# Kernel optimization log

Measured on AMD Instinct MI355X. Metric: run time of the kernel, lower is better.

## Reference

```python
import jax, jax.numpy as jnp
import numpy as np

D = 512      # node_feature_size
LAT = 768    # latent_size
B = 16       # number of graphs
S = 256      # conditioning sequence length
H = 8        # attention heads


def _ln(x, g, b):
    m = x.mean(-1, keepdims=True)
    v = jnp.var(x, axis=-1, keepdims=True)
    return (x - m) / jnp.sqrt(v + 1e-5) * g + b


def setup_inputs() -> dict:
    key = jax.random.key(0)
    ks = jax.random.split(key, 10)
    lengths = np.array([512 + 32 * i for i in range(B)])  # ragged node counts
    N = int(lengths.sum())                                # 12032
    Lmax = int(lengths.max())                             # 992
    graph_batch = jnp.asarray(np.repeat(np.arange(B), lengths), dtype=jnp.int32)
    valid = np.array([S - 8 * i for i in range(B)])
    # torch key_padding_mask semantics: True = position is ignored (padding)
    conditioning_mask = jnp.asarray(np.arange(S)[None, :] >= valid[:, None])
    p = lambda k, sh: jax.random.normal(k, sh, jnp.float32) * 0.02
    return dict(
        graph_nodes=jax.random.normal(ks[0], (N, D), jnp.float32),
        graph_batch=graph_batch,
        conditioning_vector=jax.random.normal(ks[1], (B, S, LAT), jnp.float32),
        conditioning_mask=conditioning_mask,
        max_nodes=Lmax,
        num_heads=H,
        Wq=p(ks[2], (D, D)), bq=jnp.zeros(D, jnp.float32),
        Wk=p(ks[3], (LAT, D)), bk=jnp.zeros(D, jnp.float32),
        Wv=p(ks[4], (LAT, D)), bv=jnp.zeros(D, jnp.float32),
        in_w=p(ks[5], (3, D, D)), in_b=jnp.zeros((3, D), jnp.float32),
        Wo=p(ks[6], (D, D)), bo=jnp.zeros(D, jnp.float32),
        ln1_g=jnp.ones(D, jnp.float32), ln1_b=jnp.zeros(D, jnp.float32),
        W1=p(ks[7], (D, D)), b1=jnp.zeros(D, jnp.float32),
        ln2_g=jnp.ones(D, jnp.float32), ln2_b=jnp.zeros(D, jnp.float32),
    )


def reference(graph_nodes, graph_batch, conditioning_vector, conditioning_mask,
              max_nodes, num_heads, Wq, bq, Wk, bk, Wv, bv, in_w, in_b,
              Wo, bo, ln1_g, ln1_b, W1, b1, ln2_g, ln2_b):
    N, Dm = graph_nodes.shape
    Bn, Sk, _ = conditioning_vector.shape
    dh = Dm // num_heads
    # --- pad ragged node sets to dense [B, Lmax, D] (vectorized scatter) ---
    counts = jax.ops.segment_sum(jnp.ones(N, jnp.int32), graph_batch, num_segments=Bn)
    starts = jnp.concatenate([jnp.zeros(1, jnp.int32), jnp.cumsum(counts)[:-1].astype(jnp.int32)])
    pos = jnp.arange(N, dtype=jnp.int32) - starts[graph_batch]
    dense = jnp.zeros((Bn, max_nodes, Dm), graph_nodes.dtype).at[graph_batch, pos].set(graph_nodes)
    # --- projections ---
    q = dense @ Wq + bq
    k = conditioning_vector @ Wk + bk
    v = conditioning_vector @ Wv + bv
    # --- MultiheadAttention internal in-projections ---
    qh = (q @ in_w[0] + in_b[0]).reshape(Bn, max_nodes, num_heads, dh)
    kh = (k @ in_w[1] + in_b[1]).reshape(Bn, Sk, num_heads, dh)
    vh = (v @ in_w[2] + in_b[2]).reshape(Bn, Sk, num_heads, dh)
    scores = jnp.einsum('blhd,bshd->bhls', qh, kh) / jnp.sqrt(jnp.asarray(dh, qh.dtype))
    scores = jnp.where(conditioning_mask[:, None, None, :], -jnp.inf, scores)
    attn = jax.nn.softmax(scores, axis=-1)     # [B,H,L,S]
    av_attn = attn.mean(axis=1)                # head-averaged weights [B,L,S]
    ctx = jnp.einsum('bhls,bshd->blhd', attn, vh).reshape(Bn, max_nodes, Dm)
    attn_out = ctx @ Wo + bo
    # --- residual + LN + FFN + LN (dropout inactive / eval mode) ---
    x = _ln(attn_out + dense, ln1_g, ln1_b)
    x = jax.nn.leaky_relu(x @ W1 + b1) + x     # slope 0.01 matches nn.LeakyReLU
    x = _ln(x, ln2_g, ln2_b)
    # --- unpad back to ragged [N, D] (vectorized gather) ---
    node_out = x[graph_batch, pos]
    return node_out, av_attn
```

## Files before the change

kernel.cpp:

```cpp
#include <hip/hip_runtime.h>
#include <math.h>

#define D_   512
#define LAT_ 768
#define B_   16
#define S_   256
#define H_   8
#define DH_  64

typedef __bf16 bf16x8 __attribute__((ext_vector_type(8)));
typedef float f32x4 __attribute__((ext_vector_type(4)));

__device__ __forceinline__ unsigned short f2bf(float f) {
  unsigned u = __float_as_uint(f);
  unsigned r = (u + 0x7fffu + ((u >> 16) & 1u)) >> 16;
  return (unsigned short)r;
}

__global__ void mask_canon_k(const void* __restrict__ mask, int* __restrict__ out, int n) {
  int i = blockIdx.x * blockDim.x + threadIdx.x;
  if (i >= n) return;
  const unsigned char* pb = (const unsigned char*)mask;
  const int*   pi = (const int*)mask;
  const float* pf = (const float*)mask;
  unsigned int w = ((const unsigned int*)mask)[1023];
  int v;
  if (w == 0x01010101u)      v = pb[i];
  else if (w == 0x3f800000u) v = (pf[i] != 0.0f);
  else                       v = (pi[i] != 0);
  out[i] = v ? 1 : 0;
}

__global__ void starts_k(const int* __restrict__ gb, int* __restrict__ starts, int n) {
  int i = blockIdx.x * blockDim.x + threadIdx.x;
  if (i >= n) return;
  if (i == 0 || gb[i] != gb[i - 1]) starts[gb[i]] = i;
}

__global__ __launch_bounds__(256) void scatter_k(const float* __restrict__ nodes,
    const int* __restrict__ gb, const int* __restrict__ starts,
    float* __restrict__ dense, int Lmax) {
  int i = blockIdx.x;
  int b = gb[i], p = i - starts[b];
  const float* src = nodes + (size_t)i * D_;
  float* dst = dense + ((size_t)b * Lmax + p) * D_;
  dst[threadIdx.x]       = src[threadIdx.x];
  dst[threadIdx.x + 256] = src[threadIdx.x + 256];
}

__device__ __forceinline__ void pack_chunk(const float* __restrict__ W,
    unsigned short* __restrict__ out, int K, int ntoff, int idx) {
  int n = idx & 511, kc = idx >> 9;
  int kt = kc >> 2, kblk = kc & 3;
  int nt = n >> 7, nblk = (n >> 4) & 7, col = n & 15;
  int KT = K >> 5;
  size_t ob = ((size_t)((nt + ntoff) * KT + kt) * 4096) + nblk * 512 + kblk * 128 + col * 8;
  unsigned short v[8];
#pragma unroll
  for (int j = 0; j < 8; ++j) v[j] = f2bf(W[(size_t)(kc * 8 + j) * 512 + n]);
  int4 pk;
  pk.x = v[0] | (v[1] << 16); pk.y = v[2] | (v[3] << 16);
  pk.z = v[4] | (v[5] << 16); pk.w = v[6] | (v[7] << 16);
  *(int4*)&out[ob] = pk;
}

__global__ __launch_bounds__(256) void pack1_k(const float* __restrict__ in_w,
    const float* __restrict__ Wo, const float* __restrict__ W1,
    unsigned short* iw0, unsigned short* iw1, unsigned short* iw2,
    unsigned short* Wo_pk, unsigned short* W1_pk) {
  int bid = blockIdx.x, sel = bid >> 7, within = bid & 127;
  const float* W; unsigned short* out;
  switch (sel) {
    case 0: W = in_w;               out = iw0;   break;
    case 1: W = in_w + 512 * 512;   out = iw1;   break;
    case 2: W = in_w + 2 * 512 * 512; out = iw2; break;
    case 3: W = Wo;                 out = Wo_pk; break;
    default: W = W1;                out = W1_pk; break;
  }
  pack_chunk(W, out, 512, 0, within * 256 + threadIdx.x);
}

__global__ __launch_bounds__(256) void pack2_k(const float* __restrict__ Wqp,
    const float* __restrict__ Wkp, const float* __restrict__ Wvp,
    unsigned short* Wqp_pk, unsigned short* kv_pk) {
  int bid = blockIdx.x, tid = threadIdx.x;
  if (bid < 128)      pack_chunk(Wqp, Wqp_pk, 512, 0, bid * 256 + tid);
  else if (bid < 320) pack_chunk(Wkp, kv_pk, 768, 0, (bid - 128) * 256 + tid);
  else                pack_chunk(Wvp, kv_pk, 768, 4, (bid - 320) * 256 + tid);
}

__device__ __forceinline__ void mgemm64(const float* __restrict__ A,
    const unsigned short* __restrict__ Bpk, const float* __restrict__ bias,
    float* __restrict__ C, int M, int N, int K, int xt, int yt,
    unsigned short* Al, unsigned short* Bl) {
  const int tid = threadIdx.x;
  const int lane = tid & 63, wid = tid >> 6;
  const int wr = wid >> 1, wc = wid & 1;
  const int row0 = yt * 64, col0 = xt * 128;
  const int KT = K >> 5;
  f32x4 acc[2][4];
#pragma unroll
  for (int m = 0; m < 2; ++m)
#pragma unroll
    for (int n = 0; n < 4; ++n) acc[m][n] = (f32x4){0.f, 0.f, 0.f, 0.f};
  const int kb0 = tid & 3, ar = tid >> 2;
  const unsigned short* bsrc = Bpk + (size_t)xt * KT * 4096;

  for (int kt = 0; kt < KT; ++kt) {
    {
      const unsigned short* g1 = bsrc + (size_t)kt * 4096 + wid * 512 + lane * 8;
      __builtin_amdgcn_global_load_lds(
          (const __attribute__((address_space(1))) void*)g1,
          (__attribute__((address_space(3))) void*)&Bl[wid * 512], 16, 0, 0);
      __builtin_amdgcn_global_load_lds(
          (const __attribute__((address_space(1))) void*)(g1 + 2048),
          (__attribute__((address_space(3))) void*)&Bl[2048 + wid * 512], 16, 0, 0);
    }
    {
      const float* ap = A + (size_t)(row0 + ar) * K + kt * 32 + kb0 * 8;
      float4 f0 = *(const float4*)ap;
      float4 f1 = *(const float4*)(ap + 4);
      int4 pk;
      pk.x = f2bf(f0.x) | (f2bf(f0.y) << 16);
      pk.y = f2bf(f0.z) | (f2bf(f0.w) << 16);
      pk.z = f2bf(f1.x) | (f2bf(f1.y) << 16);
      pk.w = f2bf(f1.z) | (f2bf(f1.w) << 16);
      *(int4*)&Al[(ar >> 4) * 512 + kb0 * 128 + (ar & 15) * 8] = pk;
    }
    __syncthreads();
    bf16x8 af[2], bfr[4];
#pragma unroll
    for (int m = 0; m < 2; ++m)
      af[m] = *(const bf16x8*)&Al[(wr * 2 + m) * 512 + lane * 8];
#pragma unroll
    for (int n = 0; n < 4; ++n)
      bfr[n] = *(const bf16x8*)&Bl[(wc * 4 + n) * 512 + lane * 8];
#pragma unroll
    for (int m = 0; m < 2; ++m)
#pragma unroll
      for (int n = 0; n < 4; ++n)
        acc[m][n] = __builtin_amdgcn_mfma_f32_16x16x32_bf16(af[m], bfr[n], acc[m][n], 0, 0, 0);
    __syncthreads();
  }
  const int cl = lane & 15, rg = lane >> 4;
  float bv[4];
#pragma unroll
  for (int n = 0; n < 4; ++n)
    bv[n] = bias ? bias[col0 + wc * 64 + n * 16 + cl] : 0.f;
#pragma unroll
  for (int m = 0; m < 2; ++m) {
    int r = row0 + wr * 32 + m * 16 + rg * 4;
#pragma unroll
    for (int n = 0; n < 4; ++n) {
      int c = col0 + wc * 64 + n * 16 + cl;
#pragma unroll
      for (int i = 0; i < 4; ++i)
        C[(size_t)(r + i) * N + c] = acc[m][n][i] + bv[n];
    }
  }
}

__global__ __launch_bounds__(256) void gemm64_k(const float* __restrict__ A,
    const unsigned short* __restrict__ Bpk, const float* __restrict__ bias,
    float* __restrict__ C, int M, int N, int K) {
  __shared__ __align__(16) unsigned short Al[2048];
  __shared__ __align__(16) unsigned short Bl[4096];
  mgemm64(A, Bpk, bias, C, M, N, K, blockIdx.x, blockIdx.y, Al, Bl);
}

__global__ __launch_bounds__(256) void fold_k(const float* __restrict__ Wq,
    const float* __restrict__ Wk, const float* __restrict__ Wv,
    const unsigned short* iw0, const unsigned short* iw1, const unsigned short* iw2,
    float* Wqp, float* Wkp, float* Wvp) {
  __shared__ __align__(16) unsigned short Al[2048];
  __shared__ __align__(16) unsigned short Bl[4096];
  int bid = blockIdx.x;
  if (bid < 32)       mgemm64(Wq, iw0, nullptr, Wqp, 512, 512, 512, bid & 3, bid >> 2, Al, Bl);
  else if (bid < 80)  { int r = bid - 32; mgemm64(Wk, iw1, nullptr, Wkp, 768, 512, 512, r & 3, r >> 2, Al, Bl); }
  else                { int r = bid - 80; mgemm64(Wv, iw2, nullptr, Wvp, 768, 512, 512, r & 3, r >> 2, Al, Bl); }
}

__global__ __launch_bounds__(256) void proj_k(const float* __restrict__ dense,
    const float* __restrict__ cond, const unsigned short* Wqp_pk,
    const unsigned short* kv_pk, const float* __restrict__ bqp,
    const float* __restrict__ bkv, float* qh, float* kvh, int BL) {
  __shared__ __align__(16) unsigned short Al[2048];
  __shared__ __align__(16) unsigned short Bl[4096];
  int bid = blockIdx.x;
  int nq = (BL >> 6) << 2;
  if (bid < nq)
    mgemm64(dense, Wqp_pk, bqp, qh, BL, 512, 512, bid & 3, bid >> 2, Al, Bl);
  else {
    int r = bid - nq;
    mgemm64(cond, kv_pk, bkv, kvh, B_ * S_, 1024, LAT_, r & 7, r >> 3, Al, Bl);
  }
}

__global__ void bias3_k(const float* __restrict__ bq, const float* __restrict__ bk,
    const float* __restrict__ bv, const float* __restrict__ in_w,
    const float* __restrict__ in_b, float* bqp, float* bkv) {
  int sel = blockIdx.x >> 1;
  int j = (blockIdx.x & 1) * 256 + threadIdx.x;
  const float* bin; const float* W; const float* badd; float* out;
  if (sel == 0)      { bin = bq; W = in_w;                 badd = in_b;          out = bqp; }
  else if (sel == 1) { bin = bk; W = in_w + 512 * 512;     badd = in_b + D_;     out = bkv; }
  else               { bin = bv; W = in_w + 2 * 512 * 512; badd = in_b + 2 * D_; out = bkv + 512; }
  float s = badd[j];
  for (int k = 0; k < D_; ++k) s += bin[k] * W[(size_t)k * D_ + j];
  out[j] = s;
}

__device__ __forceinline__ float rmax16(float v) {
  v = fmaxf(v, __shfl_xor(v, 1)); v = fmaxf(v, __shfl_xor(v, 2));
  v = fmaxf(v, __shfl_xor(v, 4)); v = fmaxf(v, __shfl_xor(v, 8));
  return v;
}
__device__ __forceinline__ float rsum16(float v) {
  v += __shfl_xor(v, 1); v += __shfl_xor(v, 2);
  v += __shfl_xor(v, 4); v += __shfl_xor(v, 8);
  return v;
}

__global__ __launch_bounds__(256) void attn_k(const float* __restrict__ qh,
    const float* __restrict__ kvh, const int* __restrict__ maskc,
    float* __restrict__ ctx, float* __restrict__ avout, int Lmax) {
  const int bid = blockIdx.x;
  const int b = bid & 15;
  const int l0 = (bid >> 4) * 32;
  const int tid = threadIdx.x;
  const int lane = tid & 63, w = tid >> 6;
  const int lg = lane >> 4, l15 = lane & 15;
  __shared__ __align__(16) __bf16 v_lds[256][72];
  __shared__ __align__(16) __bf16 p_lds[32][264];
  __shared__ float maxred[4][32];
  __shared__ float sumred[4][32];
  __shared__ float mask_s[S_];
  mask_s[tid] = maskc[b * S_ + tid] ? -1.0e30f : 0.f;
  __syncthreads();
  float madd[4];
#pragma unroll
  for (int n = 0; n < 4; ++n) madd[n] = mask_s[w * 64 + n * 16 + l15];

  float av[2][4][4];
#pragma unroll
  for (int m = 0; m < 2; ++m)
#pragma unroll
    for (int n = 0; n < 4; ++n)
#pragma unroll
      for (int i = 0; i < 4; ++i) av[m][n][i] = 0.f;

  const size_t qrow0 = (size_t)b * Lmax + l0;
  const int srow = tid >> 2, scol = (tid & 3) * 16;

#pragma unroll 1
  for (int h = 0; h < H_; ++h) {
    __syncthreads();
#pragma unroll
    for (int pass = 0; pass < 4; ++pass) {
      int s = pass * 64 + srow;
      const float* vp = kvh + (size_t)(b * S_ + s) * 1024 + 512 + h * DH_ + scol;
      bf16x8 t0, t1;
#pragma unroll
      for (int j = 0; j < 8; ++j) { t0[j] = (__bf16)vp[j]; t1[j] = (__bf16)vp[8 + j]; }
      *(bf16x8*)&v_lds[s][scol]     = t0;
      *(bf16x8*)&v_lds[s][scol + 8] = t1;
    }
    f32x4 qk[2][4];
#pragma unroll
    for (int m = 0; m < 2; ++m)
#pragma unroll
      for (int n = 0; n < 4; ++n) qk[m][n] = (f32x4){0.f, 0.f, 0.f, 0.f};
#pragma unroll
    for (int kt = 0; kt < 2; ++kt) {
      bf16x8 afr[2];
#pragma unroll
      for (int m = 0; m < 2; ++m) {
        const float* qp = qh + (qrow0 + m * 16 + l15) * D_ + h * DH_ + kt * 32 + lg * 8;
#pragma unroll
        for (int j = 0; j < 8; ++j) afr[m][j] = (__bf16)qp[j];
      }
#pragma unroll
      for (int n = 0; n < 4; ++n) {
        const float* kp = kvh + ((size_t)(b * S_) + w * 64 + n * 16 + l15) * 1024
                          + h * DH_ + kt * 32 + lg * 8;
        bf16x8 bfr;
#pragma unroll
        for (int j = 0; j < 8; ++j) bfr[j] = (__bf16)kp[j];
#pragma unroll
        for (int m = 0; m < 2; ++m)
          qk[m][n] = __builtin_amdgcn_mfma_f32_16x16x32_bf16(afr[m], bfr, qk[m][n], 0, 0, 0);
      }
    }
#pragma unroll
    for (int m = 0; m < 2; ++m)
#pragma unroll
      for (int n = 0; n < 4; ++n)
#pragma unroll
        for (int i = 0; i < 4; ++i)
          qk[m][n][i] = qk[m][n][i] * 0.125f + madd[n];
    float pm[2][4];
#pragma unroll
    for (int m = 0; m < 2; ++m)
#pragma unroll
      for (int i = 0; i < 4; ++i) {
        float v = fmaxf(fmaxf(qk[m][0][i], qk[m][1][i]), fmaxf(qk[m][2][i], qk[m][3][i]));
        pm[m][i] = rmax16(v);
      }
    if (l15 == 0) {
#pragma unroll
      for (int m = 0; m < 2; ++m)
#pragma unroll
        for (int i = 0; i < 4; ++i) maxred[w][m * 16 + lg * 4 + i] = pm[m][i];
    }
    __syncthreads();
    float gm[2][4], ps[2][4];
#pragma unroll
    for (int m = 0; m < 2; ++m)
#pragma unroll
      for (int i = 0; i < 4; ++i) {
        int row = m * 16 + lg * 4 + i;
        gm[m][i] = fmaxf(fmaxf(maxred[0][row], maxred[1][row]),
                         fmaxf(maxred[2][row], maxred[3][row]));
        ps[m][i] = 0.f;
      }
#pragma unroll
    for (int m = 0; m < 2; ++m)
#pragma unroll
      for (int n = 0; n < 4; ++n)
#pragma unroll
        for (int i = 0; i < 4; ++i) {
          float e = __expf(qk[m][n][i] - gm[m][i]);
          qk[m][n][i] = e;
          ps[m][i] += e;
        }
#pragma unroll
    for (int m = 0; m < 2; ++m)
#pragma unroll
      for (int i = 0; i < 4; ++i) pm[m][i] = rsum16(ps[m][i]);
    if (l15 == 0) {
#pragma unroll
      for (int m = 0; m < 2; ++m)
#pragma unroll
        for (int i = 0; i < 4; ++i) sumred[w][m * 16 + lg * 4 + i] = pm[m][i];
    }
    __syncthreads();
#pragma unroll
    for (int m = 0; m < 2; ++m)
#pragma unroll
      for (int i = 0; i < 4; ++i) {
        int row = m * 16 + lg * 4 + i;
        float inv = 1.f / (sumred[0][row] + sumred[1][row] + sumred[2][row] + sumred[3][row]);
#pragma unroll
        for (int n = 0; n < 4; ++n) {
          float p = qk[m][n][i] * inv;
          av[m][n][i] += p * 0.125f;
          p_lds[row][w * 64 + n * 16 + l15] = (__bf16)p;
        }
      }
    __syncthreads();
    f32x4 pv[2];
    pv[0] = (f32x4){0.f, 0.f, 0.f, 0.f};
    pv[1] = (f32x4){0.f, 0.f, 0.f, 0.f};
#pragma unroll
    for (int ks = 0; ks < 8; ++ks) {
      bf16x8 vb;
#pragma unroll
      for (int j = 0; j < 8; ++j) vb[j] = v_lds[ks * 32 + lg * 8 + j][w * 16 + l15];
#pragma unroll
      for (int m = 0; m < 2; ++m) {
        bf16x8 pa = *(const bf16x8*)&p_lds[m * 16 + l15][ks * 32 + lg * 8];
        pv[m] = __builtin_amdgcn_mfma_f32_16x16x32_bf16(pa, vb, pv[m], 0, 0, 0);
      }
    }
#pragma unroll
    for (int m = 0; m < 2; ++m)
#pragma unroll
      for (int i = 0; i < 4; ++i)
        ctx[(qrow0 + m * 16 + lg * 4 + i) * D_ + h * DH_ + w * 16 + l15] = pv[m][i];
  }
#pragma unroll
  for (int m = 0; m < 2; ++m)
#pragma unroll
    for (int i = 0; i < 4; ++i) {
      size_t arow = (qrow0 + m * 16 + lg * 4 + i) * S_;
#pragma unroll
      for (int n = 0; n < 4; ++n)
        avout[arow + w * 64 + n * 16 + l15] = av[m][n][i];
    }
}

__global__ __launch_bounds__(256) void ln_add_k(const float* __restrict__ a,
    const float* __restrict__ r, const float* __restrict__ g,
    const float* __restrict__ be, float* __restrict__ out) {
  size_t row = (size_t)blockIdx.x * D_;
  int tid = threadIdx.x;
  __shared__ float red[256];
  float v0 = a[row + tid]       + r[row + tid];
  float v1 = a[row + tid + 256] + r[row + tid + 256];
  red[tid] = v0 + v1;
  __syncthreads();
  for (int o = 128; o > 0; o >>= 1) { if (tid < o) red[tid] += red[tid + o]; __syncthreads(); }
  float mean = red[0] * (1.f / D_);
  __syncthreads();
  red[tid] = v0 * v0 + v1 * v1;
  __syncthreads();
  for (int o = 128; o > 0; o >>= 1) { if (tid < o) red[tid] += red[tid + o]; __syncthreads(); }
  float var = red[0] * (1.f / D_) - mean * mean;
  float rstd = rsqrtf(var + 1e-5f);
  out[row + tid]       = (v0 - mean) * rstd * g[tid]       + be[tid];
  out[row + tid + 256] = (v1 - mean) * rstd * g[tid + 256] + be[tid + 256];
}

__global__ __launch_bounds__(256) void final_k(const float* __restrict__ h1,
    const float* __restrict__ x1, const int* __restrict__ gb,
    const int* __restrict__ starts, const float* __restrict__ g,
    const float* __restrict__ be, float* __restrict__ out, int Lmax) {
  int i = blockIdx.x, tid = threadIdx.x;
  int b = gb[i], p = i - starts[b];
  size_t row = ((size_t)b * Lmax + p) * D_;
  __shared__ float red[256];
  float t0 = h1[row + tid];       t0 = (t0 >= 0.f) ? t0 : 0.01f * t0; t0 += x1[row + tid];
  float t1 = h1[row + tid + 256]; t1 = (t1 >= 0.f) ? t1 : 0.01f * t1; t1 += x1[row + tid + 256];
  red[tid] = t0 + t1;
  __syncthreads();
  for (int o = 128; o > 0; o >>= 1) { if (tid < o) red[tid] += red[tid + o]; __syncthreads(); }
  float mean = red[0] * (1.f / D_);
  __syncthreads();
  red[tid] = t0 * t0 + t1 * t1;
  __syncthreads();
  for (int o = 128; o > 0; o >>= 1) { if (tid < o) red[tid] += red[tid + o]; __syncthreads(); }
  float var = red[0] * (1.f / D_) - mean * mean;
  float rstd = rsqrtf(var + 1e-5f);
  out[(size_t)i * D_ + tid]       = (t0 - mean) * rstd * g[tid]       + be[tid];
  out[(size_t)i * D_ + tid + 256] = (t1 - mean) * rstd * g[tid + 256] + be[tid + 256];
}

extern "C" void kernel_launch(void* const* d_in, const int* in_sizes, int n_in,
                              void* d_out, int out_size, void* d_ws, size_t ws_size,
                              hipStream_t stream) {
  const float* nodes = (const float*)d_in[0];
  const int*   gb    = (const int*)d_in[1];
  const float* cond  = (const float*)d_in[2];
  const void*  maskp = d_in[3];
  const float* Wq   = (const float*)d_in[6];
  const float* bq   = (const float*)d_in[7];
  const float* Wk   = (const float*)d_in[8];
  const float* bk   = (const float*)d_in[9];
  const float* Wv   = (const float*)d_in[10];
  const float* bv   = (const float*)d_in[11];
  const float* in_w = (const float*)d_in[12];
  const float* in_b = (const float*)d_in[13];
  const float* Wo   = (const float*)d_in[14];
  const float* bo   = (const float*)d_in[15];
  const float* g1   = (const float*)d_in[16];
  const float* b1ln = (const float*)d_in[17];
  const float* W1   = (const float*)d_in[18];
  const float* b1f  = (const float*)d_in[19];
  const float* g2   = (const float*)d_in[20];
  const float* b2ln = (const float*)d_in[21];

  const int N    = in_sizes[0] / D_;
  const int Lmax = (out_size - N * D_) / (B_ * S_);
  const int BL   = B_ * Lmax;

  float* ws = (float*)d_ws;
  int* starts = (int*)(ws + 0);
  int* maskc  = (int*)(ws + 64);
  size_t o = 8192;
  float* dense = ws + o; o += (size_t)BL * D_;
  float* qh    = ws + o; o += (size_t)BL * D_;
  float* ctx   = qh;
  float* kvh   = ws + o; o += (size_t)B_ * S_ * 1024;
  float* tmp   = ws + o; o += (size_t)BL * D_;
  float* x1    = ws + o; o += (size_t)BL * D_;
  float* h1    = dense;
  float* Wqp = ws + o; o += (size_t)D_ * D_;
  float* Wkp = ws + o; o += (size_t)LAT_ * D_;
  float* Wvp = ws + o; o += (size_t)LAT_ * D_;
  float* bqp = ws + o; o += D_;
  float* bkv = ws + o; o += 1024;
  unsigned short* iw0_pk = (unsigned short*)(ws + o); o += (size_t)D_ * D_ / 2;
  unsigned short* iw1_pk = (unsigned short*)(ws + o); o += (size_t)D_ * D_ / 2;
  unsigned short* iw2_pk = (unsigned short*)(ws + o); o += (size_t)D_ * D_ / 2;
  unsigned short* Wqp_pk = (unsigned short*)(ws + o); o += (size_t)D_ * D_ / 2;
  unsigned short* kv_pk  = (unsigned short*)(ws + o); o += (size_t)LAT_ * 1024 / 2;
  unsigned short* Wo_pk  = (unsigned short*)(ws + o); o += (size_t)D_ * D_ / 2;
  unsigned short* W1_pk  = (unsigned short*)(ws + o); o += (size_t)D_ * D_ / 2;

  (void)hipMemsetAsync(d_ws, 0, (8192 + (size_t)BL * D_) * sizeof(float), stream);

  mask_canon_k<<<(B_ * S_ + 255) / 256, 256, 0, stream>>>(maskp, maskc, B_ * S_);
  starts_k<<<(N + 255) / 256, 256, 0, stream>>>(gb, starts, N);
  scatter_k<<<N, 256, 0, stream>>>(nodes, gb, starts, dense, Lmax);

  pack1_k<<<640, 256, 0, stream>>>(in_w, Wo, W1, iw0_pk, iw1_pk, iw2_pk, Wo_pk, W1_pk);
  fold_k<<<128, 256, 0, stream>>>(Wq, Wk, Wv, iw0_pk, iw1_pk, iw2_pk, Wqp, Wkp, Wvp);
  pack2_k<<<512, 256, 0, stream>>>(Wqp, Wkp, Wvp, Wqp_pk, kv_pk);
  bias3_k<<<6, 256, 0, stream>>>(bq, bk, bv, in_w, in_b, bqp, bkv);

  proj_k<<<(BL >> 6) * 4 + 512, 256, 0, stream>>>(dense, cond, Wqp_pk, kv_pk,
      bqp, bkv, qh, kvh, BL);

  attn_k<<<(Lmax / 32) * B_, 256, 0, stream>>>(qh, kvh, maskc, ctx,
      (float*)d_out + (size_t)N * D_, Lmax);

  gemm64_k<<<dim3(4, BL / 64), 256, 0, stream>>>(ctx, Wo_pk, bo, tmp, BL, D_, D_);
  ln_add_k<<<BL, 256, 0, stream>>>(tmp, dense, g1, b1ln, x1);

  gemm64_k<<<dim3(4, BL / 64), 256, 0, stream>>>(x1, W1_pk, b1f, h1, BL, D_, D_);
  final_k<<<N, 256, 0, stream>>>(h1, x1, gb, starts, g2, b2ln, (float*)d_out, Lmax);
}
```

Before: 267.0 us.

## Halve attention query tile, stage V in two register-prefetched halves

The attention kernel now handles 16 query rows per block instead of 32, which doubles the grid and cuts per-block LDS use. The V tile is loaded into registers with float4 loads before the QK MFMAs and written to LDS in two 128-row halves, with the second half prefetched while the first half's PV MFMAs run. Q and K fragment loads are vectorized to float4. In exchange, K and V are re-read from global memory twice as often across blocks, and each head loop has more barriers.

```diff
diff --git a/kernel.cpp b/kernel.cpp
--- a/kernel.cpp
+++ b/kernel.cpp
@@ -226,14 +226,14 @@
     float* __restrict__ ctx, float* __restrict__ avout, int Lmax) {
   const int bid = blockIdx.x;
   const int b = bid & 15;
-  const int l0 = (bid >> 4) * 32;
+  const int l0 = (bid >> 4) * 16;
   const int tid = threadIdx.x;
   const int lane = tid & 63, w = tid >> 6;
   const int lg = lane >> 4, l15 = lane & 15;
-  __shared__ __align__(16) __bf16 v_lds[256][72];
-  __shared__ __align__(16) __bf16 p_lds[32][264];
-  __shared__ float maxred[4][32];
-  __shared__ float sumred[4][32];
+  __shared__ __align__(16) __bf16 v_lds[128][66];
+  __shared__ __align__(16) __bf16 p_lds[16][260];
+  __shared__ float maxred[4][16];
+  __shared__ float sumred[4][16];
   __shared__ float mask_s[S_];
   mask_s[tid] = maskc[b * S_ + tid] ? -1.0e30f : 0.f;
   __syncthreads();
@@ -241,152 +241,172 @@
 #pragma unroll
   for (int n = 0; n < 4; ++n) madd[n] = mask_s[w * 64 + n * 16 + l15];
 
-  float av[2][4][4];
-#pragma unroll
-  for (int m = 0; m < 2; ++m)
-#pragma unroll
-    for (int n = 0; n < 4; ++n)
-#pragma unroll
-      for (int i = 0; i < 4; ++i) av[m][n][i] = 0.f;
+  float av[4][4];
+#pragma unroll
+  for (int n = 0; n < 4; ++n)
+#pragma unroll
+    for (int i = 0; i < 4; ++i) av[n][i] = 0.f;
 
   const size_t qrow0 = (size_t)b * Lmax + l0;
-  const int srow = tid >> 2, scol = (tid & 3) * 16;
+  const int vrow = tid >> 1, vcol0 = (tid & 1) * 32;
+  const float* vbase = kvh + (size_t)(b * S_) * 1024 + 512;
 
 #pragma unroll 1
   for (int h = 0; h < H_; ++h) {
-    __syncthreads();
-#pragma unroll
-    for (int pass = 0; pass < 4; ++pass) {
-      int s = pass * 64 + srow;
-      const float* vp = kvh + (size_t)(b * S_ + s) * 1024 + 512 + h * DH_ + scol;
-      bf16x8 t0, t1;
-#pragma unroll
-      for (int j = 0; j < 8; ++j) { t0[j] = (__bf16)vp[j]; t1[j] = (__bf16)vp[8 + j]; }
-      *(bf16x8*)&v_lds[s][scol]     = t0;
-      *(bf16x8*)&v_lds[s][scol + 8] = t1;
-    }
-    f32x4 qk[2][4];
-#pragma unroll
-    for (int m = 0; m < 2; ++m)
-#pragma unroll
-      for (int n = 0; n < 4; ++n) qk[m][n] = (f32x4){0.f, 0.f, 0.f, 0.f};
+    float4 vreg[8];
+    {
+      const float* vp = vbase + (size_t)vrow * 1024 + h * DH_ + vcol0;
+#pragma unroll
+      for (int i = 0; i < 8; ++i) vreg[i] = *(const float4*)(vp + i * 4);
+    }
+    f32x4 qk[4];
+#pragma unroll
+    for (int n = 0; n < 4; ++n) qk[n] = (f32x4){0.f, 0.f, 0.f, 0.f};
 #pragma unroll
     for (int kt = 0; kt < 2; ++kt) {
-      bf16x8 afr[2];
-#pragma unroll
-      for (int m = 0; m < 2; ++m) {
-        const float* qp = qh + (qrow0 + m * 16 + l15) * D_ + h * DH_ + kt * 32 + lg * 8;
-#pragma unroll
-        for (int j = 0; j < 8; ++j) afr[m][j] = (__bf16)qp[j];
+      bf16x8 afr;
+      {
+        const float* qp = qh + (qrow0 + l15) * D_ + h * DH_ + kt * 32 + lg * 8;
+        float4 f0 = *(const float4*)qp, f1 = *(const float4*)(qp + 4);
+        afr[0] = (__bf16)f0.x; afr[1] = (__bf16)f0.y; afr[2] = (__bf16)f0.z; afr[3] = (__bf16)f0.w;
+        afr[4] = (__bf16)f1.x; afr[5] = (__bf16)f1.y; afr[6] = (__bf16)f1.z; afr[7] = (__bf16)f1.w;
       }
 #pragma unroll
       for (int n = 0; n < 4; ++n) {
         const float* kp = kvh + ((size_t)(b * S_) + w * 64 + n * 16 + l15) * 1024
                           + h * DH_ + kt * 32 + lg * 8;
+        float4 f0 = *(const float4*)kp, f1 = *(const float4*)(kp + 4);
         bf16x8 bfr;
-#pragma unroll
-        for (int j = 0; j < 8; ++j) bfr[j] = (__bf16)kp[j];
-#pragma unroll
-        for (int m = 0; m < 2; ++m)
-          qk[m][n] = __builtin_amdgcn_mfma_f32_16x16x32_bf16(afr[m], bfr, qk[m][n], 0, 0, 0);
+        bfr[0] = (__bf16)f0.x; bfr[1] = (__bf16)f0.y; bfr[2] = (__bf16)f0.z; bfr[3] = (__bf16)f0.w;
+        bfr[4] = (__bf16)f1.x; bfr[5] = (__bf16)f1.y; bfr[6] = (__bf16)f1.z; bfr[7] = (__bf16)f1.w;
+        qk[n] = __builtin_amdgcn_mfma_f32_16x16x32_bf16(afr, bfr, qk[n], 0, 0, 0);
       }
     }
 #pragma unroll
-    for (int m = 0; m < 2; ++m)
-#pragma unroll
-      for (int n = 0; n < 4; ++n)
-#pragma unroll
-        for (int i = 0; i < 4; ++i)
-          qk[m][n][i] = qk[m][n][i] * 0.125f + madd[n];
-    float pm[2][4];
-#pragma unroll
-    for (int m = 0; m < 2; ++m)
+    for (int n = 0; n < 4; ++n)
+#pragma unroll
+      for (int i = 0; i < 4; ++i)
+        qk[n][i] = qk[n][i] * 0.125f + madd[n];
+    float pm[4];
+#pragma unroll
+    for (int i = 0; i < 4; ++i) {
+      float v = fmaxf(fmaxf(qk[0][i], qk[1][i]), fmaxf(qk[2][i], qk[3][i]));
+      pm[i] = rmax16(v);
+    }
+    if (l15 == 0) {
+#pragma unroll
+      for (int i = 0; i < 4; ++i) maxred[w][lg * 4 + i] = pm[i];
+    }
+    __syncthreads();
+    float gm[4], ps[4];
+#pragma unroll
+    for (int i = 0; i < 4; ++i) {
+      int row = lg * 4 + i;
+      gm[i] = fmaxf(fmaxf(maxred[0][row], maxred[1][row]),
+                    fmaxf(maxred[2][row], maxred[3][row]));
+      ps[i] = 0.f;
+    }
+#pragma unroll
+    for (int n = 0; n < 4; ++n)
 #pragma unroll
       for (int i = 0; i < 4; ++i) {
-        float v = fmaxf(fmaxf(qk[m][0][i], qk[m][1][i]), fmaxf(qk[m][2][i], qk[m][3][i]));
-        pm[m][i] = rmax16(v);
+        float e = __expf(qk[n][i] - gm[i]);
+        qk[n][i] = e;
+        ps[i] += e;
       }
+#pragma unroll
+    for (int i = 0; i < 4; ++i) pm[i] = rsum16(ps[i]);
     if (l15 == 0) {
 #pragma unroll
-      for (int m = 0; m < 2; ++m)
-#pragma unroll
-        for (int i = 0; i < 4; ++i) maxred[w][m * 16 + lg * 4 + i] = pm[m][i];
-    }
-    __syncthreads();
-    float gm[2][4], ps[2][4];
-#pragma unroll
-    for (int m = 0; m < 2; ++m)
-#pragma unroll
-      for (int i = 0; i < 4; ++i) {
-        int row = m * 16 + lg * 4 + i;
-        gm[m][i] = fmaxf(fmaxf(maxred[0][row], maxred[1][row]),
-                         fmaxf(maxred[2][row], maxred[3][row]));
-        ps[m][i] = 0.f;
+      for (int i = 0; i < 4; ++i) sumred[w][lg * 4 + i] = pm[i];
+    }
+    __syncthreads();
+#pragma unroll
+    for (int i = 0; i < 4; ++i) {
+      int row = lg * 4 + i;
+      float inv = 1.f / (sumred[0][row] + sumred[1][row] + sumred[2][row] + sumred[3][row]);
+#pragma unroll
+      for (int n = 0; n < 4; ++n) {
+        float p = qk[n][i] * inv;
+        av[n][i] += p * 0.125f;
+        p_lds[row][w * 64 + n * 16 + l15] = (__bf16)p;
       }
-#pragma unroll
-    for (int m = 0; m < 2; ++m)
-#pragma unroll
-      for (int n = 0; n < 4; ++n)
-#pragma unroll
-        for (int i = 0; i < 4; ++i) {
-          float e = __expf(qk[m][n][i] - gm[m][i]);
-          qk[m][n][i] = e;
-          ps[m][i] += e;
-        }
-#pragma unroll
-    for (int m = 0; m < 2; ++m)
-#pragma unroll
-      for (int i = 0; i < 4; ++i) pm[m][i] = rsum16(ps[m][i]);
-    if (l15 == 0) {
-#pragma unroll
-      for (int m = 0; m < 2; ++m)
-#pragma unroll
-        for (int i = 0; i < 4; ++i) sumred[w][m * 16 + lg * 4 + i] = pm[m][i];
-    }
-    __syncthreads();
-#pragma unroll
-    for (int m = 0; m < 2; ++m)
-#pragma unroll
-      for (int i = 0; i < 4; ++i) {
-        int row = m * 16 + lg * 4 + i;
-        float inv = 1.f / (sumred[0][row] + sumred[1][row] + sumred[2][row] + sumred[3][row]);
-#pragma unroll
-        for (int n = 0; n < 4; ++n) {
-          float p = qk[m][n][i] * inv;
-          av[m][n][i] += p * 0.125f;
-          p_lds[row][w * 64 + n * 16 + l15] = (__bf16)p;
-        }
+    }
+    {
+      bf16x8 t0, t1, t2, t3;
+#pragma unroll
+      for (int j = 0; j < 4; ++j) {
+        float4 f = vreg[j];
+        t0[j * 2 + 0] = (__bf16)f.x; t0[j * 2 + 1] = (__bf16)f.y;
       }
-    __syncthreads();
-    f32x4 pv[2];
-    pv[0] = (f32x4){0.f, 0.f, 0.f, 0.f};
-    pv[1] = (f32x4){0.f, 0.f, 0.f, 0.f};
-#pragma unroll
-    for (int ks = 0; ks < 8; ++ks) {
+      __bf16* dst = &v_lds[vrow][vcol0];
+      float* fr = (float*)vreg;
+#pragma unroll
+      for (int j = 0; j < 8; ++j) t0[j] = (__bf16)fr[j];
+#pragma unroll
+      for (int j = 0; j < 8; ++j) t1[j] = (__bf16)fr[8 + j];
+#pragma unroll
+      for (int j = 0; j < 8; ++j) t2[j] = (__bf16)fr[16 + j];
+#pragma unroll
+      for (int j = 0; j < 8; ++j) t3[j] = (__bf16)fr[24 + j];
+      *(bf16x8*)(dst)      = t0;
+      *(bf16x8*)(dst + 8)  = t1;
+      *(bf16x8*)(dst + 16) = t2;
+      *(bf16x8*)(dst + 24) = t3;
+    }
+    {
+      const float* vp = vbase + (size_t)(128 + vrow) * 1024 + h * DH_ + vcol0;
+#pragma unroll
+      for (int i = 0; i < 8; ++i) vreg[i] = *(const float4*)(vp + i * 4);
+    }
+    __syncthreads();
+    f32x4 pv = (f32x4){0.f, 0.f, 0.f, 0.f};
+#pragma unroll
+    for (int ks = 0; ks < 4; ++ks) {
       bf16x8 vb;
 #pragma unroll
       for (int j = 0; j < 8; ++j) vb[j] = v_lds[ks * 32 + lg * 8 + j][w * 16 + l15];
-#pragma unroll
-      for (int m = 0; m < 2; ++m) {
-        bf16x8 pa = *(const bf16x8*)&p_lds[m * 16 + l15][ks * 32 + lg * 8];
-        pv[m] = __builtin_amdgcn_mfma_f32_16x16x32_bf16(pa, vb, pv[m], 0, 0, 0);
-      }
-    }
-#pragma unroll
-    for (int m = 0; m < 2; ++m)
-#pragma unroll
-      for (int i = 0; i < 4; ++i)
-        ctx[(qrow0 + m * 16 + lg * 4 + i) * D_ + h * DH_ + w * 16 + l15] = pv[m][i];
+      bf16x8 pa = *(const bf16x8*)&p_lds[l15][ks * 32 + lg * 8];
+      pv = __builtin_amdgcn_mfma_f32_16x16x32_bf16(pa, vb, pv, 0, 0, 0);
+    }
+    __syncthreads();
+    {
+      bf16x8 t0, t1, t2, t3;
+      float* fr = (float*)vreg;
+#pragma unroll
+      for (int j = 0; j < 8; ++j) t0[j] = (__bf16)fr[j];
+#pragma unroll
+      for (int j = 0; j < 8; ++j) t1[j] = (__bf16)fr[8 + j];
+#pragma unroll
+      for (int j = 0; j < 8; ++j) t2[j] = (__bf16)fr[16 + j];
+#pragma unroll
+      for (int j = 0; j < 8; ++j) t3[j] = (__bf16)fr[24 + j];
+      __bf16* dst = &v_lds[vrow][vcol0];
+      *(bf16x8*)(dst)      = t0;
+      *(bf16x8*)(dst + 8)  = t1;
+      *(bf16x8*)(dst + 16) = t2;
+      *(bf16x8*)(dst + 24) = t3;
+    }
+    __syncthreads();
+#pragma unroll
+    for (int ks = 4; ks < 8; ++ks) {
+      bf16x8 vb;
+#pragma unroll
+      for (int j = 0; j < 8; ++j) vb[j] = v_lds[(ks - 4) * 32 + lg * 8 + j][w * 16 + l15];
+      bf16x8 pa = *(const bf16x8*)&p_lds[l15][ks * 32 + lg * 8];
+      pv = __builtin_amdgcn_mfma_f32_16x16x32_bf16(pa, vb, pv, 0, 0, 0);
+    }
+#pragma unroll
+    for (int i = 0; i < 4; ++i)
+      ctx[(qrow0 + lg * 4 + i) * D_ + h * DH_ + w * 16 + l15] = pv[i];
   }
 #pragma unroll
-  for (int m = 0; m < 2; ++m)
-#pragma unroll
-    for (int i = 0; i < 4; ++i) {
-      size_t arow = (qrow0 + m * 16 + lg * 4 + i) * S_;
-#pragma unroll
-      for (int n = 0; n < 4; ++n)
-        avout[arow + w * 64 + n * 16 + l15] = av[m][n][i];
-    }
+  for (int i = 0; i < 4; ++i) {
+    size_t arow = (qrow0 + lg * 4 + i) * S_;
+#pragma unroll
+    for (int n = 0; n < 4; ++n)
+      avout[arow + w * 64 + n * 16 + l15] = av[n][i];
+  }
 }
 
 __global__ __launch_bounds__(256) void ln_add_k(const float* __restrict__ a,
@@ -501,7 +521,7 @@
   proj_k<<<(BL >> 6) * 4 + 512, 256, 0, stream>>>(dense, cond, Wqp_pk, kv_pk,
       bqp, bkv, qh, kvh, BL);
 
-  attn_k<<<(Lmax / 32) * B_, 256, 0, stream>>>(qh, kvh, maskc, ctx,
+  attn_k<<<(Lmax / 16) * B_, 256, 0, stream>>>(qh, kvh, maskc, ctx,
       (float*)d_out + (size_t)N * D_, Lmax);
 
   gemm64_k<<<dim3(4, BL / 64), 256, 0, stream>>>(ctx, Wo_pk, bo, tmp, BL, D_, D_);
```

New measurement: 340.3 us. +27.4%, slower.
